# Optimization experiments

Hardware: AMD Instinct MI355X
Metric: run time of the kernel (lower is better)

## Reference

```python
import jax, jax.numpy as jnp
import numpy as np


def setup_inputs() -> dict:
    key = jax.random.key(0)
    ks = jax.random.split(key, 8)
    B, N, F = 16, 2048, 128
    x = jax.random.normal(ks[0], (B, N, F), dtype=jnp.float32)
    # dense (pre-normalized) adjacency, as spektral GCNConv expects normalized A
    a = jax.random.uniform(ks[1], (B, N, N), dtype=jnp.float32) / N
    w1 = jax.random.normal(ks[2], (F, 32), dtype=jnp.float32) * 0.1
    b1 = jnp.zeros((32,), dtype=jnp.float32)
    w2 = jax.random.normal(ks[3], (32, 32), dtype=jnp.float32) * 0.1
    b2 = jnp.zeros((32,), dtype=jnp.float32)
    wf1 = jax.random.normal(ks[4], (32, 512), dtype=jnp.float32) * 0.1
    bf1 = jnp.zeros((512,), dtype=jnp.float32)
    wf2 = jax.random.normal(ks[5], (512, 1), dtype=jnp.float32) * 0.1
    bf2 = jnp.zeros((1,), dtype=jnp.float32)
    return {"x": x, "a": a, "w1": w1, "b1": b1, "w2": w2, "b2": b2,
            "wf1": wf1, "bf1": bf1, "wf2": wf2, "bf2": bf2}


def _gcn(x, a, w, b):
    # GCNConv: elu(A_norm @ X @ W + b)
    h = jnp.einsum('bnf,fc->bnc', x, w)   # dense transform first (cheaper)
    h = jnp.einsum('bnm,bmc->bnc', a, h)  # adjacency aggregation
    return jax.nn.elu(h + b)


def reference(x, a, w1, b1, w2, b2, wf1, bf1, wf2, bf2):
    h = _gcn(x, a, w1, b1)                # [B,N,32]
    h = _gcn(h, a, w2, b2)                # [B,N,32]
    pooled = jnp.sum(h, axis=1)           # GlobalSumPool -> [B,32]
    h = jax.nn.relu(pooled @ wf1 + bf1)   # [B,512]
    out = jax.nn.sigmoid(h @ wf2 + bf2)   # [B,1]
    return out
```

## Files before the change

### kernel.cpp

```cpp
#include <hip/hip_runtime.h>
#include <hip/hip_bf16.h>
#include <math.h>

#define BATCH 16
#define NN 2048
#define FF 128
#define CC 32
#define HID 512
#define QM 512
#define LSTR 520
#define KS1 128

typedef float v4f __attribute__((ext_vector_type(4)));
typedef float v2f __attribute__((ext_vector_type(2)));
typedef short short8 __attribute__((ext_vector_type(8)));
typedef short s4v __attribute__((ext_vector_type(4)));

__device__ __forceinline__ unsigned short f2bf(float f) {
  unsigned u = __float_as_uint(f);
  u += 0x7fffu + ((u >> 16) & 1u);
  return (unsigned short)(u >> 16);
}

__device__ __forceinline__ float elu1(float x) {
  return x > 0.f ? x : expm1f(x);
}

__global__ __launch_bounds__(256)
void k_xw1(const float* __restrict__ src, const float* __restrict__ w,
           unsigned short* __restrict__ outT) {
  int t = threadIdx.x;
  int wv = t >> 6, l = t & 63, lo = l & 15, q = l >> 4;
  int rowt = blockIdx.x * 4 + wv;
  long row = (long)rowt * 16 + lo;

  short8 wf[FF / 32][2];
#pragma unroll
  for (int kc = 0; kc < FF / 32; ++kc)
#pragma unroll
    for (int h = 0; h < 2; ++h) {
      short8 f;
#pragma unroll
      for (int j = 0; j < 8; ++j)
        f[j] = (short)f2bf(w[(kc * 32 + q * 8 + j) * CC + h * 16 + lo]);
      wf[kc][h] = f;
    }

  v4f acc0 = {0.f, 0.f, 0.f, 0.f}, acc1 = {0.f, 0.f, 0.f, 0.f};
#pragma unroll
  for (int kc = 0; kc < FF / 32; ++kc) {
    const float* sp = src + row * FF + kc * 32 + q * 8;
    float4 a0 = *(const float4*)sp;
    float4 a1 = *(const float4*)(sp + 4);
    short8 af;
    af[0] = (short)f2bf(a0.x); af[1] = (short)f2bf(a0.y);
    af[2] = (short)f2bf(a0.z); af[3] = (short)f2bf(a0.w);
    af[4] = (short)f2bf(a1.x); af[5] = (short)f2bf(a1.y);
    af[6] = (short)f2bf(a1.z); af[7] = (short)f2bf(a1.w);
    acc0 = __builtin_amdgcn_mfma_f32_16x16x32_bf16(af, wf[kc][0], acc0, 0, 0, 0);
    acc1 = __builtin_amdgcn_mfma_f32_16x16x32_bf16(af, wf[kc][1], acc1, 0, 0, 0);
  }

  int b = rowt >> 7;
  int nbase = (rowt & 127) * 16;
#pragma unroll
  for (int r = 0; r < 4; ++r) {
    int n = nbase + q * 4 + r;
    outT[((long)b * CC + lo) * NN + n] = f2bf(acc0[r]);
    outT[((long)b * CC + 16 + lo) * NN + n] = f2bf(acc1[r]);
  }
}

__global__ __launch_bounds__(256, 2)
void k_agg1(const float* __restrict__ a, unsigned char* __restrict__ afp8,
            const unsigned short* __restrict__ hT, float* __restrict__ hpart) {
  __shared__ __attribute__((aligned(16))) unsigned short hs[CC * LSTR];
  __shared__ __attribute__((aligned(16))) unsigned short at[2][64 * KS1];

  int t = threadIdx.x;
  int bid = blockIdx.x;
  int rt = bid & 31, qm = (bid >> 5) & 3, b = bid >> 7;
  int n0 = rt * 64;

  int r0 = t >> 5, chunk = t & 31;
  const float* ga = a + ((long)(b * NN + n0 + r0)) * NN + qm * QM + chunk * 4;
  unsigned char* gao = afp8 + ((long)(b * NN + n0 + r0)) * NN + qm * QM + chunk * 4;
  int swb = r0 * 256 + ((chunk * 8) ^ (r0 << 4));

  float4 ar[8];
  const float sc = 1024.f;

#pragma unroll
  for (int j = 0; j < 8; ++j)
    ar[j] = *(const float4*)(ga + (long)j * 8 * NN);

#pragma unroll
  for (int i = 0; i < 8; ++i) {
    int jj = i * 256 + t;
    int c = jj >> 6, off = (jj & 63) * 8;
    *(uint4*)&hs[c * LSTR + off] =
        *(const uint4*)(hT + ((long)b * CC + c) * NN + qm * QM + off);
  }

#pragma unroll
  for (int j = 0; j < 8; ++j) {
    char* lp = (char*)&at[0][0] + swb + j * 2048;
    s4v bv;
    bv[0] = (short)f2bf(ar[j].x); bv[1] = (short)f2bf(ar[j].y);
    bv[2] = (short)f2bf(ar[j].z); bv[3] = (short)f2bf(ar[j].w);
    *(s4v*)lp = bv;
    int w0 = __builtin_amdgcn_cvt_pk_fp8_f32(ar[j].x * sc, ar[j].y * sc, 0, false);
    w0 = __builtin_amdgcn_cvt_pk_fp8_f32(ar[j].z * sc, ar[j].w * sc, w0, true);
    *(int*)(gao + (long)j * 8 * NN) = w0;
  }
  __syncthreads();

  int l = t & 63, wv = t >> 6, lo = l & 15, q = l >> 4;
  int lrow = wv * 16 + lo;
  const unsigned short* h0 = &hs[lo * LSTR + q * 8];

  v4f acc0 = {0.f, 0.f, 0.f, 0.f}, acc1 = {0.f, 0.f, 0.f, 0.f};

#pragma unroll
  for (int ks = 0; ks < 4; ++ks) {
    if (ks < 3) {
#pragma unroll
      for (int j = 0; j < 8; ++j)
        ar[j] = *(const float4*)(ga + (long)j * 8 * NN + (ks + 1) * KS1);
    }
    const char* ab = (const char*)at + (ks & 1) * (64 * KS1 * 2);
#pragma unroll
    for (int kk = 0; kk < 4; ++kk) {
      short8 af = *(const short8*)(ab + lrow * 256 + ((q * 16 + kk * 64) ^ ((lo & 7) << 4)));
      int m = ks * KS1 + kk * 32;
      short8 b0 = *(const short8*)(h0 + m);
      short8 b1 = *(const short8*)(h0 + 16 * LSTR + m);
      acc0 = __builtin_amdgcn_mfma_f32_16x16x32_bf16(af, b0, acc0, 0, 0, 0);
      acc1 = __builtin_amdgcn_mfma_f32_16x16x32_bf16(af, b1, acc1, 0, 0, 0);
    }
    if (ks < 3) {
      char* lb = (char*)&at[(ks + 1) & 1][0];
#pragma unroll
      for (int j = 0; j < 8; ++j) {
        char* lp = lb + swb + j * 2048;
        s4v bv;
        bv[0] = (short)f2bf(ar[j].x); bv[1] = (short)f2bf(ar[j].y);
        bv[2] = (short)f2bf(ar[j].z); bv[3] = (short)f2bf(ar[j].w);
        *(s4v*)lp = bv;
        int w0 = __builtin_amdgcn_cvt_pk_fp8_f32(ar[j].x * sc, ar[j].y * sc, 0, false);
        w0 = __builtin_amdgcn_cvt_pk_fp8_f32(ar[j].z * sc, ar[j].w * sc, w0, true);
        *(int*)(gao + (long)j * 8 * NN + (ks + 1) * KS1) = w0;
      }
      __syncthreads();
    }
  }

  float* op = hpart + ((long)qm * BATCH * NN + (long)b * NN) * CC;
#pragma unroll
  for (int r = 0; r < 4; ++r) {
    int n = n0 + wv * 16 + q * 4 + r;
    op[(long)n * CC + lo] = acc0[r];
    op[(long)n * CC + 16 + lo] = acc1[r];
  }
}

__global__ __launch_bounds__(256)
void k_xw2(const float* __restrict__ h1p, const float* __restrict__ b1,
           const float* __restrict__ w2, unsigned short* __restrict__ outT) {
  const long QS = (long)BATCH * NN * CC;
  int t = threadIdx.x;
  int wv = t >> 6, l = t & 63, lo = l & 15, q = l >> 4;
  int rowt = blockIdx.x * 4 + wv;
  long row = (long)rowt * 16 + lo;

  short8 wf[2];
#pragma unroll
  for (int h = 0; h < 2; ++h) {
    short8 f;
#pragma unroll
    for (int j = 0; j < 8; ++j)
      f[j] = (short)f2bf(w2[(q * 8 + j) * CC + h * 16 + lo]);
    wf[h] = f;
  }

  const float* p = h1p + row * CC + q * 8;
  float s[8] = {0, 0, 0, 0, 0, 0, 0, 0};
#pragma unroll
  for (int qq = 0; qq < 4; ++qq) {
    float4 u0 = *(const float4*)(p + qq * QS);
    float4 u1 = *(const float4*)(p + qq * QS + 4);
    s[0] += u0.x; s[1] += u0.y; s[2] += u0.z; s[3] += u0.w;
    s[4] += u1.x; s[5] += u1.y; s[6] += u1.z; s[7] += u1.w;
  }
  short8 af;
#pragma unroll
  for (int j = 0; j < 8; ++j)
    af[j] = (short)f2bf(elu1(s[j] + b1[q * 8 + j]));

  v4f acc0 = {0.f, 0.f, 0.f, 0.f}, acc1 = {0.f, 0.f, 0.f, 0.f};
  acc0 = __builtin_amdgcn_mfma_f32_16x16x32_bf16(af, wf[0], acc0, 0, 0, 0);
  acc1 = __builtin_amdgcn_mfma_f32_16x16x32_bf16(af, wf[1], acc1, 0, 0, 0);

  const float inv = 1.f / 1024.f;
  int b = rowt >> 7;
  int nbase = (rowt & 127) * 16;
#pragma unroll
  for (int r = 0; r < 4; ++r) {
    int n = nbase + q * 4 + r;
    outT[((long)b * CC + lo) * NN + n] = f2bf(acc0[r] * inv);
    outT[((long)b * CC + 16 + lo) * NN + n] = f2bf(acc1[r] * inv);
  }
}

__global__ __launch_bounds__(256, 2)
void k_agg2(const unsigned char* __restrict__ afp8,
            const unsigned short* __restrict__ hT, float* __restrict__ hpart) {
  __shared__ __attribute__((aligned(16))) unsigned short hs[CC * LSTR];
  __shared__ __attribute__((aligned(16))) unsigned char a2[64 * QM];

  int t = threadIdx.x;
  int bid = blockIdx.x;
  int rt = bid & 31, qm = (bid >> 5) & 3, b = bid >> 7;
  int n0 = rt * 64;

  int r0 = t >> 5, chunk = t & 31;
  const unsigned char* ga =
      afp8 + ((long)(b * NN + n0 + r0)) * NN + qm * QM + chunk * 16;
  char* lw = (char*)a2 + r0 * 512 + ((chunk * 16) ^ (r0 << 4));

  uint4 arr[8];
#pragma unroll
  for (int j = 0; j < 8; ++j)
    arr[j] = *(const uint4*)(ga + (long)j * 8 * NN);

#pragma unroll
  for (int i = 0; i < 8; ++i) {
    int jj = i * 256 + t;
    int c = jj >> 6, off = (jj & 63) * 8;
    *(uint4*)&hs[c * LSTR + off] =
        *(const uint4*)(hT + ((long)b * CC + c) * NN + qm * QM + off);
  }

#pragma unroll
  for (int j = 0; j < 8; ++j)
    *(uint4*)(lw + j * 4096) = arr[j];
  __syncthreads();

  int l = t & 63, wv = t >> 6, lo = l & 15, q = l >> 4;
  int lrow = wv * 16 + lo;
  const unsigned short* h0 = &hs[lo * LSTR + q * 8];
  const char* ab = (const char*)a2;

  v4f acc0 = {0.f, 0.f, 0.f, 0.f}, acc1 = {0.f, 0.f, 0.f, 0.f};
#pragma unroll
  for (int kk = 0; kk < 16; ++kk) {
    int2 av = *(const int2*)(ab + lrow * 512 + ((q * 8 + kk * 32) ^ ((lo & 7) << 4)));
    v2f f01 = __builtin_amdgcn_cvt_pk_f32_fp8(av.x, false);
    v2f f23 = __builtin_amdgcn_cvt_pk_f32_fp8(av.x, true);
    v2f f45 = __builtin_amdgcn_cvt_pk_f32_fp8(av.y, false);
    v2f f67 = __builtin_amdgcn_cvt_pk_f32_fp8(av.y, true);
    short8 af;
    af[0] = (short)f2bf(f01.x); af[1] = (short)f2bf(f01.y);
    af[2] = (short)f2bf(f23.x); af[3] = (short)f2bf(f23.y);
    af[4] = (short)f2bf(f45.x); af[5] = (short)f2bf(f45.y);
    af[6] = (short)f2bf(f67.x); af[7] = (short)f2bf(f67.y);
    int m = kk * 32;
    short8 b0 = *(const short8*)(h0 + m);
    short8 b1 = *(const short8*)(h0 + 16 * LSTR + m);
    acc0 = __builtin_amdgcn_mfma_f32_16x16x32_bf16(af, b0, acc0, 0, 0, 0);
    acc1 = __builtin_amdgcn_mfma_f32_16x16x32_bf16(af, b1, acc1, 0, 0, 0);
  }

  float* op = hpart + ((long)qm * BATCH * NN + (long)b * NN) * CC;
#pragma unroll
  for (int r = 0; r < 4; ++r) {
    int n = n0 + wv * 16 + q * 4 + r;
    op[(long)n * CC + lo] = acc0[r];
    op[(long)n * CC + 16 + lo] = acc1[r];
  }
}

__global__ __launch_bounds__(256)
void k_pool(const float* __restrict__ h2p, const float* __restrict__ b2,
            float* __restrict__ pp) {
  const long QS = (long)BATCH * NN * CC;
  __shared__ float red[8][CC + 1];
  int t = threadIdx.x;
  int b = blockIdx.x >> 3, seg = blockIdx.x & 7;
  int c = t & 31, nl = t >> 5;
  float bc = b2[c];
  float s = 0.f;
  for (int n = seg * 256 + nl; n < seg * 256 + 256; n += 8) {
    long idx = ((long)b * NN + n) * CC + c;
    s += elu1(h2p[idx] + h2p[QS + idx] + h2p[2 * QS + idx] + h2p[3 * QS + idx] + bc);
  }
  red[nl][c] = s;
  __syncthreads();
  if (nl < 4) red[nl][c] += red[nl + 4][c];
  __syncthreads();
  if (nl < 2) red[nl][c] += red[nl + 2][c];
  __syncthreads();
  if (nl == 0) pp[((long)seg * BATCH + b) * CC + c] = red[0][c] + red[1][c];
}

__global__ __launch_bounds__(512)
void k5_mlp(const float* __restrict__ pp, const float* __restrict__ wf1,
            const float* __restrict__ bf1, const float* __restrict__ wf2,
            const float* __restrict__ bf2, float* __restrict__ out) {
  __shared__ float red[HID];
  __shared__ float ps[CC];
  int b = blockIdx.x, j = threadIdx.x;
  if (j < CC) {
    float s = 0.f;
#pragma unroll
    for (int g = 0; g < 8; ++g) s += pp[((long)g * BATCH + b) * CC + j];
    ps[j] = s;
  }
  __syncthreads();
  float acc = bf1[j];
#pragma unroll
  for (int c = 0; c < CC; ++c) acc += ps[c] * wf1[c * HID + j];
  red[j] = fmaxf(acc, 0.f) * wf2[j];
  __syncthreads();
  for (int s = HID / 2; s > 0; s >>= 1) {
    if (j < s) red[j] += red[j + s];
    __syncthreads();
  }
  if (j == 0) out[b] = 1.f / (1.f + expf(-(red[0] + bf2[0])));
}

extern "C" void kernel_launch(void* const* d_in, const int* in_sizes, int n_in,
                              void* d_out, int out_size, void* d_ws, size_t ws_size,
                              hipStream_t stream) {
  const float* x   = (const float*)d_in[0];
  const float* a   = (const float*)d_in[1];
  const float* w1  = (const float*)d_in[2];
  const float* b1  = (const float*)d_in[3];
  const float* w2  = (const float*)d_in[4];
  const float* b2  = (const float*)d_in[5];
  const float* wf1 = (const float*)d_in[6];
  const float* bf1 = (const float*)d_in[7];
  const float* wf2 = (const float*)d_in[8];
  const float* bf2 = (const float*)d_in[9];
  float* out = (float*)d_out;

  char* ws = (char*)d_ws;
  unsigned char*  afp8 = (unsigned char*)ws;
  unsigned short* hT1  = (unsigned short*)(ws + 0x4000000UL);
  unsigned short* hT2  = (unsigned short*)(ws + 0x4200000UL);
  float* h1p = (float*)(ws + 0x4400000UL);
  float* h2p = (float*)(ws + 0x5400000UL);
  float* pp  = (float*)(ws + 0x6400000UL);

  k_xw1<<<512, 256, 0, stream>>>(x, w1, hT1);
  k_agg1<<<2048, 256, 0, stream>>>(a, afp8, hT1, h1p);
  k_xw2<<<512, 256, 0, stream>>>(h1p, b1, w2, hT2);
  k_agg2<<<2048, 256, 0, stream>>>(afp8, hT2, h2p);
  k_pool<<<128, 256, 0, stream>>>(h2p, b2, pp);
  k5_mlp<<<BATCH, HID, 0, stream>>>(pp, wf1, bf1, wf2, bf2, out);
}
```

Baseline: 431.5 us.

## Drop split-K in aggregation kernels and fuse bias/ELU and pooling epilogues

Both aggregation kernels now loop over the full 2048-wide K dimension in one block instead of splitting it into four quarter partials. The node-feature tile in shared memory is reloaded for each quarter. This removes the fp32 partial-sum buffers and their reduction. Bias+ELU is applied directly in the first aggregation's epilogue. The second aggregation performs ELU and a per-block sum pool, which eliminates the separate pool kernel. In exchange, the grid shrinks from 2048 to 512 blocks and adds extra barriers, with less latency hiding (the agg2 reload is not double-buffered).

New measurement: 438.1 us. About the same (+1.5%).

```diff
diff --git a/kernel.cpp b/kernel.cpp
--- a/kernel.cpp
+++ b/kernel.cpp
@@ -72,19 +72,20 @@
 }
 
 __global__ __launch_bounds__(256, 2)
-void k_agg1(const float* __restrict__ a, unsigned char* __restrict__ afp8,
-            const unsigned short* __restrict__ hT, float* __restrict__ hpart) {
+void k_agg1f(const float* __restrict__ a, unsigned char* __restrict__ afp8,
+             const unsigned short* __restrict__ hT, const float* __restrict__ b1,
+             float* __restrict__ h1) {
   __shared__ __attribute__((aligned(16))) unsigned short hs[CC * LSTR];
   __shared__ __attribute__((aligned(16))) unsigned short at[2][64 * KS1];
 
   int t = threadIdx.x;
   int bid = blockIdx.x;
-  int rt = bid & 31, qm = (bid >> 5) & 3, b = bid >> 7;
+  int rt = bid & 31, b = bid >> 5;
   int n0 = rt * 64;
 
   int r0 = t >> 5, chunk = t & 31;
-  const float* ga = a + ((long)(b * NN + n0 + r0)) * NN + qm * QM + chunk * 4;
-  unsigned char* gao = afp8 + ((long)(b * NN + n0 + r0)) * NN + qm * QM + chunk * 4;
+  const float* ga = a + ((long)(b * NN + n0 + r0)) * NN + chunk * 4;
+  unsigned char* gao = afp8 + ((long)(b * NN + n0 + r0)) * NN + chunk * 4;
   int swb = r0 * 256 + ((chunk * 8) ^ (r0 << 4));
 
   float4 ar[8];
@@ -99,7 +100,7 @@
     int jj = i * 256 + t;
     int c = jj >> 6, off = (jj & 63) * 8;
     *(uint4*)&hs[c * LSTR + off] =
-        *(const uint4*)(hT + ((long)b * CC + c) * NN + qm * QM + off);
+        *(const uint4*)(hT + ((long)b * CC + c) * NN + off);
   }
 
 #pragma unroll
@@ -121,25 +122,26 @@
 
   v4f acc0 = {0.f, 0.f, 0.f, 0.f}, acc1 = {0.f, 0.f, 0.f, 0.f};
 
-#pragma unroll
-  for (int ks = 0; ks < 4; ++ks) {
-    if (ks < 3) {
+  for (int step = 0; step < 16; ++step) {
+    if (step < 15) {
 #pragma unroll
       for (int j = 0; j < 8; ++j)
-        ar[j] = *(const float4*)(ga + (long)j * 8 * NN + (ks + 1) * KS1);
-    }
-    const char* ab = (const char*)at + (ks & 1) * (64 * KS1 * 2);
+        ar[j] = *(const float4*)(ga + (long)j * 8 * NN + (step + 1) * KS1);
+    }
+    const char* ab = (const char*)at + (step & 1) * (64 * KS1 * 2);
+    int mloc = (step & 3) * KS1;
 #pragma unroll
     for (int kk = 0; kk < 4; ++kk) {
-      short8 af = *(const short8*)(ab + lrow * 256 + ((q * 16 + kk * 64) ^ ((lo & 7) << 4)));
-      int m = ks * KS1 + kk * 32;
+      short8 af = *(const short8*)(ab + lrow * 256 +
+                                   ((q * 16 + kk * 64) ^ ((lo & 7) << 4)));
+      int m = mloc + kk * 32;
       short8 b0 = *(const short8*)(h0 + m);
-      short8 b1 = *(const short8*)(h0 + 16 * LSTR + m);
+      short8 b1v = *(const short8*)(h0 + 16 * LSTR + m);
       acc0 = __builtin_amdgcn_mfma_f32_16x16x32_bf16(af, b0, acc0, 0, 0, 0);
-      acc1 = __builtin_amdgcn_mfma_f32_16x16x32_bf16(af, b1, acc1, 0, 0, 0);
-    }
-    if (ks < 3) {
-      char* lb = (char*)&at[(ks + 1) & 1][0];
+      acc1 = __builtin_amdgcn_mfma_f32_16x16x32_bf16(af, b1v, acc1, 0, 0, 0);
+    }
+    if (step < 15) {
+      char* lb = (char*)&at[(step + 1) & 1][0];
 #pragma unroll
       for (int j = 0; j < 8; ++j) {
         char* lp = lb + swb + j * 2048;
@@ -149,25 +151,35 @@
         *(s4v*)lp = bv;
         int w0 = __builtin_amdgcn_cvt_pk_fp8_f32(ar[j].x * sc, ar[j].y * sc, 0, false);
         w0 = __builtin_amdgcn_cvt_pk_fp8_f32(ar[j].z * sc, ar[j].w * sc, w0, true);
-        *(int*)(gao + (long)j * 8 * NN + (ks + 1) * KS1) = w0;
+        *(int*)(gao + (long)j * 8 * NN + (step + 1) * KS1) = w0;
       }
       __syncthreads();
-    }
-  }
-
-  float* op = hpart + ((long)qm * BATCH * NN + (long)b * NN) * CC;
+      if ((step & 3) == 3) {
+        int qm = (step >> 2) + 1;
+#pragma unroll
+        for (int i = 0; i < 8; ++i) {
+          int jj = i * 256 + t;
+          int c = jj >> 6, off = (jj & 63) * 8;
+          *(uint4*)&hs[c * LSTR + off] =
+              *(const uint4*)(hT + ((long)b * CC + c) * NN + qm * QM + off);
+        }
+        __syncthreads();
+      }
+    }
+  }
+
+  float* hp = h1 + (long)b * NN * CC;
 #pragma unroll
   for (int r = 0; r < 4; ++r) {
     int n = n0 + wv * 16 + q * 4 + r;
-    op[(long)n * CC + lo] = acc0[r];
-    op[(long)n * CC + 16 + lo] = acc1[r];
+    hp[(long)n * CC + lo] = elu1(acc0[r] + b1[lo]);
+    hp[(long)n * CC + 16 + lo] = elu1(acc1[r] + b1[16 + lo]);
   }
 }
 
 __global__ __launch_bounds__(256)
-void k_xw2(const float* __restrict__ h1p, const float* __restrict__ b1,
-           const float* __restrict__ w2, unsigned short* __restrict__ outT) {
-  const long QS = (long)BATCH * NN * CC;
+void k_xw2(const float* __restrict__ h1, const float* __restrict__ w2,
+           unsigned short* __restrict__ outT) {
   int t = threadIdx.x;
   int wv = t >> 6, l = t & 63, lo = l & 15, q = l >> 4;
   int rowt = blockIdx.x * 4 + wv;
@@ -183,19 +195,14 @@
     wf[h] = f;
   }
 
-  const float* p = h1p + row * CC + q * 8;
-  float s[8] = {0, 0, 0, 0, 0, 0, 0, 0};
-#pragma unroll
-  for (int qq = 0; qq < 4; ++qq) {
-    float4 u0 = *(const float4*)(p + qq * QS);
-    float4 u1 = *(const float4*)(p + qq * QS + 4);
-    s[0] += u0.x; s[1] += u0.y; s[2] += u0.z; s[3] += u0.w;
-    s[4] += u1.x; s[5] += u1.y; s[6] += u1.z; s[7] += u1.w;
-  }
+  const float* p = h1 + row * CC + q * 8;
+  float4 u0 = *(const float4*)p;
+  float4 u1 = *(const float4*)(p + 4);
   short8 af;
-#pragma unroll
-  for (int j = 0; j < 8; ++j)
-    af[j] = (short)f2bf(elu1(s[j] + b1[q * 8 + j]));
+  af[0] = (short)f2bf(u0.x); af[1] = (short)f2bf(u0.y);
+  af[2] = (short)f2bf(u0.z); af[3] = (short)f2bf(u0.w);
+  af[4] = (short)f2bf(u1.x); af[5] = (short)f2bf(u1.y);
+  af[6] = (short)f2bf(u1.z); af[7] = (short)f2bf(u1.w);
 
   v4f acc0 = {0.f, 0.f, 0.f, 0.f}, acc1 = {0.f, 0.f, 0.f, 0.f};
   acc0 = __builtin_amdgcn_mfma_f32_16x16x32_bf16(af, wf[0], acc0, 0, 0, 0);
@@ -213,34 +220,33 @@
 }
 
 __global__ __launch_bounds__(256, 2)
-void k_agg2(const unsigned char* __restrict__ afp8,
-            const unsigned short* __restrict__ hT, float* __restrict__ hpart) {
+void k_agg2f(const unsigned char* __restrict__ afp8,
+             const unsigned short* __restrict__ hT, const float* __restrict__ b2,
+             float* __restrict__ pp2) {
   __shared__ __attribute__((aligned(16))) unsigned short hs[CC * LSTR];
   __shared__ __attribute__((aligned(16))) unsigned char a2[64 * QM];
+  __shared__ float red[4][CC];
 
   int t = threadIdx.x;
   int bid = blockIdx.x;
-  int rt = bid & 31, qm = (bid >> 5) & 3, b = bid >> 7;
+  int rt = bid & 31, b = bid >> 5;
   int n0 = rt * 64;
 
   int r0 = t >> 5, chunk = t & 31;
-  const unsigned char* ga =
-      afp8 + ((long)(b * NN + n0 + r0)) * NN + qm * QM + chunk * 16;
+  const unsigned char* ga = afp8 + ((long)(b * NN + n0 + r0)) * NN + chunk * 16;
   char* lw = (char*)a2 + r0 * 512 + ((chunk * 16) ^ (r0 << 4));
 
   uint4 arr[8];
 #pragma unroll
   for (int j = 0; j < 8; ++j)
     arr[j] = *(const uint4*)(ga + (long)j * 8 * NN);
-
 #pragma unroll
   for (int i = 0; i < 8; ++i) {
     int jj = i * 256 + t;
     int c = jj >> 6, off = (jj & 63) * 8;
     *(uint4*)&hs[c * LSTR + off] =
-        *(const uint4*)(hT + ((long)b * CC + c) * NN + qm * QM + off);
-  }
-
+        *(const uint4*)(hT + ((long)b * CC + c) * NN + off);
+  }
 #pragma unroll
   for (int j = 0; j < 8; ++j)
     *(uint4*)(lw + j * 4096) = arr[j];
@@ -252,59 +258,71 @@
   const char* ab = (const char*)a2;
 
   v4f acc0 = {0.f, 0.f, 0.f, 0.f}, acc1 = {0.f, 0.f, 0.f, 0.f};
-#pragma unroll
-  for (int kk = 0; kk < 16; ++kk) {
-    int2 av = *(const int2*)(ab + lrow * 512 + ((q * 8 + kk * 32) ^ ((lo & 7) << 4)));
-    v2f f01 = __builtin_amdgcn_cvt_pk_f32_fp8(av.x, false);
-    v2f f23 = __builtin_amdgcn_cvt_pk_f32_fp8(av.x, true);
-    v2f f45 = __builtin_amdgcn_cvt_pk_f32_fp8(av.y, false);
-    v2f f67 = __builtin_amdgcn_cvt_pk_f32_fp8(av.y, true);
-    short8 af;
-    af[0] = (short)f2bf(f01.x); af[1] = (short)f2bf(f01.y);
-    af[2] = (short)f2bf(f23.x); af[3] = (short)f2bf(f23.y);
-    af[4] = (short)f2bf(f45.x); af[5] = (short)f2bf(f45.y);
-    af[6] = (short)f2bf(f67.x); af[7] = (short)f2bf(f67.y);
-    int m = kk * 32;
-    short8 b0 = *(const short8*)(h0 + m);
-    short8 b1 = *(const short8*)(h0 + 16 * LSTR + m);
-    acc0 = __builtin_amdgcn_mfma_f32_16x16x32_bf16(af, b0, acc0, 0, 0, 0);
-    acc1 = __builtin_amdgcn_mfma_f32_16x16x32_bf16(af, b1, acc1, 0, 0, 0);
-  }
-
-  float* op = hpart + ((long)qm * BATCH * NN + (long)b * NN) * CC;
+
+  for (int qm = 0; qm < 4; ++qm) {
+    if (qm < 3) {
+#pragma unroll
+      for (int j = 0; j < 8; ++j)
+        arr[j] = *(const uint4*)(ga + (long)j * 8 * NN + (qm + 1) * QM);
+    }
+#pragma unroll
+    for (int kk = 0; kk < 16; ++kk) {
+      int2 av = *(const int2*)(ab + lrow * 512 +
+                               ((q * 8 + kk * 32) ^ ((lo & 7) << 4)));
+      v2f f01 = __builtin_amdgcn_cvt_pk_f32_fp8(av.x, false);
+      v2f f23 = __builtin_amdgcn_cvt_pk_f32_fp8(av.x, true);
+      v2f f45 = __builtin_amdgcn_cvt_pk_f32_fp8(av.y, false);
+      v2f f67 = __builtin_amdgcn_cvt_pk_f32_fp8(av.y, true);
+      short8 af;
+      af[0] = (short)f2bf(f01.x); af[1] = (short)f2bf(f01.y);
+      af[2] = (short)f2bf(f23.x); af[3] = (short)f2bf(f23.y);
+      af[4] = (short)f2bf(f45.x); af[5] = (short)f2bf(f45.y);
+      af[6] = (short)f2bf(f67.x); af[7] = (short)f2bf(f67.y);
+      int m = kk * 32;
+      short8 b0 = *(const short8*)(h0 + m);
+      short8 b1v = *(const short8*)(h0 + 16 * LSTR + m);
+      acc0 = __builtin_amdgcn_mfma_f32_16x16x32_bf16(af, b0, acc0, 0, 0, 0);
+      acc1 = __builtin_amdgcn_mfma_f32_16x16x32_bf16(af, b1v, acc1, 0, 0, 0);
+    }
+    if (qm < 3) {
+      __syncthreads();
+#pragma unroll
+      for (int j = 0; j < 8; ++j)
+        *(uint4*)(lw + j * 4096) = arr[j];
+      int nq = qm + 1;
+#pragma unroll
+      for (int i = 0; i < 8; ++i) {
+        int jj = i * 256 + t;
+        int c = jj >> 6, off = (jj & 63) * 8;
+        *(uint4*)&hs[c * LSTR + off] =
+            *(const uint4*)(hT + ((long)b * CC + c) * NN + nq * QM + off);
+      }
+      __syncthreads();
+    }
+  }
+
+  float s0 = 0.f, s1 = 0.f;
+  float bc0 = b2[lo], bc1 = b2[16 + lo];
 #pragma unroll
   for (int r = 0; r < 4; ++r) {
-    int n = n0 + wv * 16 + q * 4 + r;
-    op[(long)n * CC + lo] = acc0[r];
-    op[(long)n * CC + 16 + lo] = acc1[r];
-  }
-}
-
-__global__ __launch_bounds__(256)
-void k_pool(const float* __restrict__ h2p, const float* __restrict__ b2,
-            float* __restrict__ pp) {
-  const long QS = (long)BATCH * NN * CC;
-  __shared__ float red[8][CC + 1];
-  int t = threadIdx.x;
-  int b = blockIdx.x >> 3, seg = blockIdx.x & 7;
-  int c = t & 31, nl = t >> 5;
-  float bc = b2[c];
-  float s = 0.f;
-  for (int n = seg * 256 + nl; n < seg * 256 + 256; n += 8) {
-    long idx = ((long)b * NN + n) * CC + c;
-    s += elu1(h2p[idx] + h2p[QS + idx] + h2p[2 * QS + idx] + h2p[3 * QS + idx] + bc);
-  }
-  red[nl][c] = s;
-  __syncthreads();
-  if (nl < 4) red[nl][c] += red[nl + 4][c];
-  __syncthreads();
-  if (nl < 2) red[nl][c] += red[nl + 2][c];
-  __syncthreads();
-  if (nl == 0) pp[((long)seg * BATCH + b) * CC + c] = red[0][c] + red[1][c];
+    s0 += elu1(acc0[r] + bc0);
+    s1 += elu1(acc1[r] + bc1);
+  }
+  s0 += __shfl_xor(s0, 16); s0 += __shfl_xor(s0, 32);
+  s1 += __shfl_xor(s1, 16); s1 += __shfl_xor(s1, 32);
+  if (l < 16) {
+    red[wv][lo] = s0;
+    red[wv][16 + lo] = s1;
+  }
+  __syncthreads();
+  if (t < CC) {
+    float p = red[0][t] + red[1][t] + red[2][t] + red[3][t];
+    pp2[((long)b * 32 + rt) * CC + t] = p;
+  }
 }
 
 __global__ __launch_bounds__(512)
-void k5_mlp(const float* __restrict__ pp, const float* __restrict__ wf1,
+void k5_mlp(const float* __restrict__ pp2, const float* __restrict__ wf1,
             const float* __restrict__ bf1, const float* __restrict__ wf2,
             const float* __restrict__ bf2, float* __restrict__ out) {
   __shared__ float red[HID];
@@ -313,7 +331,7 @@
   if (j < CC) {
     float s = 0.f;
 #pragma unroll
-    for (int g = 0; g < 8; ++g) s += pp[((long)g * BATCH + b) * CC + j];
+    for (int rt = 0; rt < 32; ++rt) s += pp2[((long)b * 32 + rt) * CC + j];
     ps[j] = s;
   }
   __syncthreads();
@@ -348,14 +366,12 @@
   unsigned char*  afp8 = (unsigned char*)ws;
   unsigned short* hT1  = (unsigned short*)(ws + 0x4000000UL);
   unsigned short* hT2  = (unsigned short*)(ws + 0x4200000UL);
-  float* h1p = (float*)(ws + 0x4400000UL);
-  float* h2p = (float*)(ws + 0x5400000UL);
-  float* pp  = (float*)(ws + 0x6400000UL);
+  float* h1  = (float*)(ws + 0x4400000UL);
+  float* pp2 = (float*)(ws + 0x4800000UL);
 
   k_xw1<<<512, 256, 0, stream>>>(x, w1, hT1);
-  k_agg1<<<2048, 256, 0, stream>>>(a, afp8, hT1, h1p);
-  k_xw2<<<512, 256, 0, stream>>>(h1p, b1, w2, hT2);
-  k_agg2<<<2048, 256, 0, stream>>>(afp8, hT2, h2p);
-  k_pool<<<128, 256, 0, stream>>>(h2p, b2, pp);
-  k5_mlp<<<BATCH, HID, 0, stream>>>(pp, wf1, bf1, wf2, bf2, out);
-}
+  k_agg1f<<<512, 256, 0, stream>>>(a, afp8, hT1, b1, h1);
+  k_xw2<<<512, 256, 0, stream>>>(h1, w2, hT2);
+  k_agg2f<<<512, 256, 0, stream>>>(afp8, hT2, b2, pp2);
+  k5_mlp<<<BATCH, HID, 0, stream>>>(pp2, wf1, bf1, wf2, bf2, out);
+}
```
